# Performance work log

Hardware: AMD Instinct MI355X
Metric: run time of the kernel (lower is better)

## Reference

```python
import jax, jax.numpy as jnp
import numpy as np

N = 200000      # nodes per graph
E = 6400000     # edges per graph
F_IN = 100      # node feature dim (GCNConv(100,16))
HID = 16
NC = 2
STRIDE = 20     # log_softmax(...)[::20]
M = N // STRIDE # rows fed to the MLP head


def _gcn(x, src, dst, W1, b1, W2, b2):
    """PyG-style GCNConv x2: add self loops, sym-normalize, linear -> aggregate -> bias."""
    n = x.shape[0]
    loops = jnp.arange(n)
    s = jnp.concatenate([src, loops])
    d = jnp.concatenate([dst, loops])
    deg = jax.ops.segment_sum(jnp.ones(s.shape[0], dtype=x.dtype), d, num_segments=n)
    dinv = jnp.where(deg > 0, jax.lax.rsqrt(deg), 0.0)
    norm = (dinv[s] * dinv[d])[:, None]  # [E+n, 1]
    h = x @ W1                                    # [n, 16]
    h = jax.ops.segment_sum(norm * h[s], d, num_segments=n) + b1
    h = jax.nn.relu(h)  # dropout is identity in eval mode
    h = h @ W2                                    # [n, 2]
    h = jax.ops.segment_sum(norm * h[s], d, num_segments=n) + b2
    return jax.nn.log_softmax(h, axis=1)[::STRIDE]  # [n/20, 2]


def setup_inputs() -> dict:
    key = jax.random.key(0)
    ks = jax.random.split(key, 24)
    inp = {
        'batch1_edge_index': jax.random.randint(ks[0], (2, E), 0, N),
        'batch1_x': jax.random.normal(ks[1], (N, F_IN), dtype=jnp.float32),
        'batch2_edge_index': jax.random.randint(ks[2], (2, E), 0, N),
        'batch2_x': jax.random.normal(ks[3], (N, F_IN), dtype=jnp.float32),
        'transE_input': jax.random.uniform(ks[4], (M,), dtype=jnp.float32),
        'ComplEx_input': jax.random.uniform(ks[5], (M,), dtype=jnp.float32),
        'path_input': jax.random.uniform(ks[6], (M,), dtype=jnp.float32),
        'edit_input': jax.random.uniform(ks[7], (M,), dtype=jnp.float32),
    }
    s = 0.1
    inp['gh_W1'] = jax.random.normal(ks[8], (F_IN, HID), dtype=jnp.float32) * s
    inp['gh_b1'] = jnp.zeros((HID,), dtype=jnp.float32)
    inp['gh_W2'] = jax.random.normal(ks[9], (HID, NC), dtype=jnp.float32) * s
    inp['gh_b2'] = jnp.zeros((NC,), dtype=jnp.float32)
    inp['gt_W1'] = jax.random.normal(ks[10], (F_IN, HID), dtype=jnp.float32) * s
    inp['gt_b1'] = jnp.zeros((HID,), dtype=jnp.float32)
    inp['gt_W2'] = jax.random.normal(ks[11], (HID, NC), dtype=jnp.float32) * s
    inp['gt_b2'] = jnp.zeros((NC,), dtype=jnp.float32)
    inp['m_W1'] = jax.random.normal(ks[12], (5, 80), dtype=jnp.float32) * s
    inp['m_b1'] = jnp.zeros((80,), dtype=jnp.float32)
    inp['m_W2'] = jax.random.normal(ks[13], (80, 10), dtype=jnp.float32) * s
    inp['m_b2'] = jnp.zeros((10,), dtype=jnp.float32)
    inp['m_W3'] = jax.random.normal(ks[14], (10, 1), dtype=jnp.float32) * s
    inp['m_b3'] = jnp.zeros((1,), dtype=jnp.float32)
    return inp


def reference(batch1_edge_index, batch1_x, batch2_edge_index, batch2_x,
              transE_input, ComplEx_input, path_input, edit_input,
              gh_W1, gh_b1, gh_W2, gh_b2,
              gt_W1, gt_b1, gt_W2, gt_b2,
              m_W1, m_b1, m_W2, m_b2, m_W3, m_b3):
    gcnh_out = _gcn(batch1_x, batch1_edge_index[0], batch1_edge_index[1],
                    gh_W1, gh_b1, gh_W2, gh_b2)
    # gcnt_out is computed in the original forward but never used in the output
    gcnt_out = _gcn(batch2_x, batch2_edge_index[0], batch2_edge_index[1],
                    gt_W1, gt_b1, gt_W2, gt_b2)
    BP_input = jnp.concatenate(
        [transE_input[:, None], ComplEx_input[:, None], path_input[:, None], gcnh_out], axis=1)  # [M, 5]
    # NOTE: original computes mean/std normalization then OVERWRITES it with
    # min_max_normalize(BP_input); we faithfully apply only global min-max.
    mn, mx = jnp.min(BP_input), jnp.max(BP_input)
    BP_norm = (BP_input - mn) / (mx - mn)
    h = jax.nn.relu(BP_norm @ m_W1 + m_b1)
    h = jax.nn.relu(h @ m_W2 + m_b2)
    out = jax.nn.sigmoid(h @ m_W3 + m_b3)  # [M, 1]
    return out
```

## Files before the change

kernel.cpp:

```cpp
#include <hip/hip_runtime.h>
#include <math.h>

#define NN 200000
#define NE 6400000
#define FIN 100
#define MR 10000
#define BSH 14
#define NBK 13
#define NSB 1563
#define EPB 4096
#define STCAP 6144

static __device__ __forceinline__ unsigned enc_f(float f){
  unsigned u = __float_as_uint(f);
  return (u & 0x80000000u) ? ~u : (u | 0x80000000u);
}
static __device__ __forceinline__ float dec_f(unsigned u){
  return (u & 0x80000000u) ? __uint_as_float(u ^ 0x80000000u) : __uint_as_float(~u);
}
static __device__ __forceinline__ unsigned short f2bf(float f){
  unsigned u = __float_as_uint(f);
  return (unsigned short)((u + 0x7fffu + ((u >> 16) & 1u)) >> 16);
}
static __device__ __forceinline__ float bf2f(unsigned short h){
  return __uint_as_float(((unsigned)h) << 16);
}

__global__ void k_init(int* bcnt2, float* gacc, unsigned* mm){
  int i = blockIdx.x*blockDim.x + threadIdx.x;
  if(i < NSB) bcnt2[i] = 0;
  if(i < 2*MR) gacc[i] = 0.f;
  if(i == 0){ mm[0] = 0xFFFFFFFFu; mm[1] = 0u; }
}

__global__ __launch_bounds__(256) void k_hist(const int4* __restrict__ dst4,
                                              int* __restrict__ bcnt2){
  __shared__ int sh[NSB];
  for(int i=threadIdx.x;i<NSB;i+=256) sh[i]=0;
  __syncthreads();
  const int nq = NE/4;
  for(int q = blockIdx.x*256 + threadIdx.x; q < nq; q += gridDim.x*256){
    int4 d = dst4[q];
    atomicAdd(&sh[d.x>>7],1); atomicAdd(&sh[d.y>>7],1);
    atomicAdd(&sh[d.z>>7],1); atomicAdd(&sh[d.w>>7],1);
  }
  __syncthreads();
  for(int i=threadIdx.x;i<NSB;i+=256){ int v=sh[i]; if(v) atomicAdd(&bcnt2[i],v); }
}

__global__ void k_scan2(const int* __restrict__ bcnt2, int* bbase2, int* bcur2,
                        int* bbase1, int* bcur1){
  __shared__ int part[256];
  int t = threadIdx.x;
  int base = t*7;
  int loc[7]; int s = 0;
  #pragma unroll
  for(int j=0;j<7;j++){ int i = base+j; loc[j] = (i<NSB)? bcnt2[i] : 0; s += loc[j]; }
  part[t] = s; __syncthreads();
  for(int o=1;o<256;o<<=1){
    int x = (t>=o)? part[t-o] : 0;
    __syncthreads();
    part[t] += x;
    __syncthreads();
  }
  int run = part[t] - s;
  #pragma unroll
  for(int j=0;j<7;j++){
    int i = base+j;
    if(i<NSB){ bbase2[i] = run; bcur2[i] = run; }
    run += loc[j];
  }
  if(t==0) bbase2[NSB] = NE;
  __syncthreads();
  if(t < NBK){ int v = bbase2[t*128]; bbase1[t] = v; bcur1[t] = v; }
  if(t == NBK){ bbase1[NBK] = NE; }
}

__global__ __launch_bounds__(256) void k_stageA(const int* __restrict__ src,
                                                const int* __restrict__ dst,
                                                int* __restrict__ bcur1,
                                                unsigned* __restrict__ bucket1){
  __shared__ unsigned stage[EPB];
  __shared__ unsigned char binOf[EPB];
  __shared__ int cnt[NBK], bst[NBK], gbase[NBK];
  int t = threadIdx.x;
  int ebase = blockIdx.x*EPB;
  int nEdge = min(EPB, NE - ebase);
  if(t < NBK) cnt[t] = 0;
  __syncthreads();
  unsigned pk[16]; int bb[16], rr[16];
  const int4* s4 = (const int4*)(src + ebase);
  const int4* d4 = (const int4*)(dst + ebase);
  #pragma unroll
  for(int j=0;j<4;j++){
    int q = t + j*256, eo = q*4;
    if(eo < nEdge){
      int4 s = s4[q]; int4 d = d4[q];
      int ds[4] = {d.x,d.y,d.z,d.w}, ss[4] = {s.x,s.y,s.z,s.w};
      #pragma unroll
      for(int k=0;k<4;k++){
        int b = ds[k]>>BSH;
        pk[j*4+k] = ((unsigned)(ds[k] & 16383) << 18) | (unsigned)ss[k];
        bb[j*4+k] = b;
        rr[j*4+k] = atomicAdd(&cnt[b], 1);
      }
    } else {
      rr[j*4+0]=rr[j*4+1]=rr[j*4+2]=rr[j*4+3] = -1;
    }
  }
  __syncthreads();
  if(t == 0){
    int run = 0;
    #pragma unroll
    for(int b=0;b<NBK;b++){ bst[b] = run; run += cnt[b]; }
  }
  __syncthreads();
  if(t < NBK && cnt[t]) gbase[t] = atomicAdd(&bcur1[t], cnt[t]);
  #pragma unroll
  for(int j=0;j<16;j++){
    if(rr[j] >= 0){
      int p = bst[bb[j]] + rr[j];
      stage[p] = pk[j]; binOf[p] = (unsigned char)bb[j];
    }
  }
  __syncthreads();
  for(int k=t; k<nEdge; k+=256){
    int b = binOf[k];
    bucket1[gbase[b] + (k - bst[b])] = stage[k];
  }
}

__global__ __launch_bounds__(256) void k_stageB(const unsigned* __restrict__ bucket1,
                                                const int* __restrict__ bbase1,
                                                int* __restrict__ bcur2,
                                                unsigned* __restrict__ bucket2){
  __shared__ unsigned stage[EPB];
  __shared__ unsigned char binOf[EPB];
  __shared__ int cnt[256], bst[256], gbase[256];
  __shared__ int bb1[NBK+1];
  int t = threadIdx.x;
  int ebase = blockIdx.x*EPB;
  int nEdge = min(EPB, NE - ebase);
  if(t < NBK) bb1[t] = bbase1[t];
  if(t == NBK) bb1[NBK] = NE;
  cnt[t] = 0;
  __syncthreads();
  int bF = 0;
  while(bF < NBK-1 && bb1[bF+1] <= ebase) bF++;
  int sb0 = bF << 7;
  unsigned pk[16]; int ln[16], rr[16];
  const uint4* e4 = (const uint4*)(bucket1 + ebase);
  int b = bF;
  #pragma unroll
  for(int j=0;j<4;j++){
    int q = t + j*256, eo = q*4;
    if(eo < nEdge){
      uint4 e = e4[q];
      unsigned ev[4] = {e.x, e.y, e.z, e.w};
      #pragma unroll
      for(int k=0;k<4;k++){
        int gidx = ebase + eo + k;
        while(b < NBK-1 && bb1[b+1] <= gidx) b++;
        unsigned p = ev[k];
        unsigned dl14 = p >> 18;
        int sbl = ((b<<7) | (int)(dl14>>7)) - sb0;
        pk[j*4+k] = ((dl14 & 127u) << 18) | (p & 0x3FFFFu);
        ln[j*4+k] = sbl;
        rr[j*4+k] = atomicAdd(&cnt[sbl], 1);
      }
    } else {
      rr[j*4+0]=rr[j*4+1]=rr[j*4+2]=rr[j*4+3] = -1;
    }
  }
  __syncthreads();
  if(t == 0){
    int run = 0;
    for(int i=0;i<256;i++){ bst[i] = run; run += cnt[i]; }
  }
  __syncthreads();
  {
    int sbg = sb0 + t;
    if(cnt[t] && sbg < NSB) gbase[t] = atomicAdd(&bcur2[sbg], cnt[t]);
  }
  #pragma unroll
  for(int j=0;j<16;j++){
    if(rr[j] >= 0){
      int p = bst[ln[j]] + rr[j];
      stage[p] = pk[j]; binOf[p] = (unsigned char)ln[j];
    }
  }
  __syncthreads();
  for(int k=t; k<nEdge; k+=256){
    int bin = binOf[k];
    bucket2[gbase[bin] + (k - bst[bin])] = stage[k];
  }
}

__global__ __launch_bounds__(256) void k_cnt(const unsigned* __restrict__ bucket2,
                                             const int* __restrict__ bbase2,
                                             float* __restrict__ dinv){
  __shared__ int c[128];
  int sb = blockIdx.x, t = threadIdx.x;
  if(t < 128) c[t] = 0;
  __syncthreads();
  int e0 = bbase2[sb], e1 = bbase2[sb+1];
  for(int i=e0+t; i<e1; i+=256){
    unsigned pkv = bucket2[i];
    atomicAdd(&c[pkv>>18], 1);
  }
  __syncthreads();
  if(t < 128){
    int g = sb*128 + t;
    if(g < NN) dinv[g] = rsqrtf((float)(c[t] + 1));
  }
}

__global__ __launch_bounds__(256) void k_xw1(const float* __restrict__ x,
                                             const float* __restrict__ W1,
                                             const float* __restrict__ dinv,
                                             unsigned short* __restrict__ h1b){
  int row = blockIdx.x*256 + threadIdx.x;
  if(row >= NN) return;
  const float4* xr = (const float4*)(x + (size_t)row*FIN);
  float acc[16];
  #pragma unroll
  for(int c=0;c<16;c++) acc[c] = 0.f;
  #pragma unroll 5
  for(int kk=0;kk<25;kk++){
    float4 xv = xr[kk];
    const float* w = W1 + kk*4*16;
    #pragma unroll
    for(int c=0;c<16;c++){
      acc[c] += xv.x*w[c] + xv.y*w[16+c] + xv.z*w[32+c] + xv.w*w[48+c];
    }
  }
  float dv = dinv[row];
  unsigned p[8];
  #pragma unroll
  for(int c=0;c<8;c++){
    p[c] = (unsigned)f2bf(acc[2*c]*dv) | ((unsigned)f2bf(acc[2*c+1]*dv) << 16);
  }
  uint4* o = (uint4*)(h1b + (size_t)row*16);
  o[0] = make_uint4(p[0],p[1],p[2],p[3]);
  o[1] = make_uint4(p[4],p[5],p[6],p[7]);
}

__global__ __launch_bounds__(512) void k_aggfused(const unsigned* __restrict__ bucket2,
                                                  const int* __restrict__ bbase2,
                                                  const float* __restrict__ dinv,
                                                  const unsigned short* __restrict__ h1b,
                                                  const float* __restrict__ b1,
                                                  const float* __restrict__ W2,
                                                  float* __restrict__ h2s){
  __shared__ unsigned srt[STCAP];
  __shared__ int cnt[128], coff[129], cur[128];
  __shared__ int wsum0;
  int t = threadIdx.x, sb = blockIdx.x;
  int e0 = bbase2[sb], e1 = bbase2[sb+1];
  int n  = e1 - e0;
  bool ok = (n <= STCAP);
  int grp = t>>4, f = t&15;
  if(t < 128) cnt[t] = 0;
  __syncthreads();

  if(ok){
    for(int i=e0+t; i<e1; i+=512) atomicAdd(&cnt[bucket2[i]>>18], 1);
    __syncthreads();
    int v = (t<128) ? cnt[t] : 0;
    int s = v;
    #pragma unroll
    for(int o=1;o<64;o<<=1){
      int u = __shfl_up(s, o, 64);
      if((t&63) >= o) s += u;
    }
    if(t == 63) wsum0 = s;
    __syncthreads();
    if(t < 128){
      int ex = s - v + ((t>=64) ? wsum0 : 0);
      coff[t] = ex; cur[t] = ex;
    }
    if(t == 0) coff[128] = n;
    __syncthreads();
    for(int i=e0+t; i<e1; i+=512){
      unsigned pkv = bucket2[i];
      int p = atomicAdd(&cur[pkv>>18], 1);
      srt[p] = pkv & 0x3FFFFu;
    }
    __syncthreads();
    for(int nd=grp; nd<128; nd+=32){
      int g = sb*128 + nd;
      if(g >= NN) continue;
      int s0 = coff[nd], s1 = coff[nd+1];
      float acc = bf2f(h1b[(size_t)g*16 + f]);
      int j = s0;
      for(; j+4 <= s1; j+=4){
        unsigned a0=srt[j], a1=srt[j+1], a2=srt[j+2], a3=srt[j+3];
        float x0 = bf2f(h1b[a0*16 + f]);
        float x1 = bf2f(h1b[a1*16 + f]);
        float x2 = bf2f(h1b[a2*16 + f]);
        float x3 = bf2f(h1b[a3*16 + f]);
        acc += (x0+x1) + (x2+x3);
      }
      for(; j<s1; j++) acc += bf2f(h1b[srt[j]*16 + f]);
      float dvd = dinv[g];
      float r = fmaxf(dvd*acc + b1[f], 0.f);
      float p0 = r * W2[f*2+0];
      float p1 = r * W2[f*2+1];
      #pragma unroll
      for(int o=8;o>0;o>>=1){
        p0 += __shfl_xor(p0, o, 16);
        p1 += __shfl_xor(p1, o, 16);
      }
      if(f == 0){
        h2s[g*2+0] = dvd * p0;
        h2s[g*2+1] = dvd * p1;
      }
    }
  } else {
    float* accf = (float*)srt;
    for(int i=t; i<2048; i+=512) accf[i] = 0.f;
    __syncthreads();
    for(int i=e0+grp; i<e1; i+=32){
      unsigned pkv = bucket2[i];
      atomicAdd(&accf[(pkv>>18)*16 + f], bf2f(h1b[(pkv & 0x3FFFFu)*16 + f]));
    }
    __syncthreads();
    for(int nd=grp; nd<128; nd+=32){
      int g = sb*128 + nd;
      if(g >= NN) continue;
      float dvd = dinv[g];
      float acc = accf[nd*16 + f] + bf2f(h1b[(size_t)g*16 + f]);
      float r = fmaxf(dvd*acc + b1[f], 0.f);
      float p0 = r * W2[f*2+0];
      float p1 = r * W2[f*2+1];
      #pragma unroll
      for(int o=8;o>0;o>>=1){
        p0 += __shfl_xor(p0, o, 16);
        p1 += __shfl_xor(p1, o, 16);
      }
      if(f == 0){
        h2s[g*2+0] = dvd * p0;
        h2s[g*2+1] = dvd * p1;
      }
    }
  }
}

__global__ __launch_bounds__(256) void k_agg2e(const unsigned* __restrict__ bucket2,
                                               const int* __restrict__ bbase2,
                                               const float* __restrict__ h2s,
                                               float* __restrict__ gacc){
  int sb = blockIdx.x, t = threadIdx.x;
  int e0 = bbase2[sb], e1 = bbase2[sb+1];
  int base = sb*128;
  for(int i=e0+t; i<e1; i+=256){
    unsigned pkv = bucket2[i];
    int g = base + (int)(pkv >> 18);
    if(g % 20 == 0){
      int srcn = (int)(pkv & 0x3FFFFu);
      int idx = g / 20;
      atomicAdd(&gacc[idx*2+0], h2s[srcn*2+0]);
      atomicAdd(&gacc[idx*2+1], h2s[srcn*2+1]);
    }
  }
}

__global__ __launch_bounds__(256) void k_post(const float* __restrict__ gacc,
                                              const float* __restrict__ h2s,
                                              const float* __restrict__ dinv,
                                              const float* __restrict__ b2,
                                              const float* __restrict__ t1,
                                              const float* __restrict__ t2,
                                              const float* __restrict__ t3,
                                              float* __restrict__ gout,
                                              unsigned* __restrict__ mm){
  int i = blockIdx.x*256 + threadIdx.x;
  float lo = 3.4e38f, hi = -3.4e38f;
  if(i < MR){
    int g = i*20;
    float dvd = dinv[g];
    float o0 = dvd*(gacc[i*2+0] + h2s[g*2+0]) + b2[0];
    float o1 = dvd*(gacc[i*2+1] + h2s[g*2+1]) + b2[1];
    float m = fmaxf(o0, o1);
    float lse = m + logf(expf(o0-m) + expf(o1-m));
    float g0 = o0 - lse, g1 = o1 - lse;
    gout[i*2+0] = g0; gout[i*2+1] = g1;
    float a = t1[i], bb = t2[i], c = t3[i];
    lo = fminf(fminf(a,bb), fminf(c, fminf(g0,g1)));
    hi = fmaxf(fmaxf(a,bb), fmaxf(c, fmaxf(g0,g1)));
  }
  #pragma unroll
  for(int o=32;o>0;o>>=1){
    lo = fminf(lo, __shfl_xor(lo, o, 64));
    hi = fmaxf(hi, __shfl_xor(hi, o, 64));
  }
  __shared__ float slo[4], shi[4];
  int w = threadIdx.x >> 6, l = threadIdx.x & 63;
  if(l == 0){ slo[w] = lo; shi[w] = hi; }
  __syncthreads();
  if(threadIdx.x == 0){
    for(int j=1;j<4;j++){ lo = fminf(lo, slo[j]); hi = fmaxf(hi, shi[j]); }
    atomicMin(&mm[0], enc_f(lo));
    atomicMax(&mm[1], enc_f(hi));
  }
}

__global__ __launch_bounds__(256) void k_mlp(const float* __restrict__ t1, const float* __restrict__ t2,
                                             const float* __restrict__ t3, const float* __restrict__ g,
                                             const unsigned* __restrict__ mm,
                                             const float* __restrict__ W1, const float* __restrict__ b1,
                                             const float* __restrict__ W2, const float* __restrict__ b2,
                                             const float* __restrict__ W3, const float* __restrict__ b3,
                                             float* __restrict__ out){
  int i = blockIdx.x*256 + threadIdx.x;
  if(i >= MR) return;
  float mn = dec_f(mm[0]), mx = dec_f(mm[1]);
  float sc = 1.f/(mx - mn);
  float in[5];
  in[0] = (t1[i]   - mn)*sc;
  in[1] = (t2[i]   - mn)*sc;
  in[2] = (t3[i]   - mn)*sc;
  in[3] = (g[2*i]  - mn)*sc;
  in[4] = (g[2*i+1]- mn)*sc;
  float a[80];
  #pragma unroll
  for(int j=0;j<80;j++){
    float s = b1[j];
    #pragma unroll
    for(int k=0;k<5;k++) s += in[k]*W1[k*80+j];
    a[j] = fmaxf(s, 0.f);
  }
  float h[10];
  #pragma unroll
  for(int j=0;j<10;j++){
    float s = b2[j];
    #pragma unroll
    for(int k=0;k<80;k++) s += a[k]*W2[k*10+j];
    h[j] = fmaxf(s, 0.f);
  }
  float o = b3[0];
  #pragma unroll
  for(int k=0;k<10;k++) o += h[k]*W3[k];
  out[i] = 1.f/(1.f + expf(-o));
}

extern "C" void kernel_launch(void* const* d_in, const int* in_sizes, int n_in,
                              void* d_out, int out_size, void* d_ws, size_t ws_size,
                              hipStream_t stream) {
  (void)in_sizes; (void)n_in; (void)out_size; (void)ws_size;
  const int*   eidx    = (const int*)  d_in[0];
  const int*   src     = eidx;
  const int*   dst     = eidx + NE;
  const int4*  dst4    = (const int4*) dst;
  const float* x       = (const float*)d_in[1];
  const float* transE  = (const float*)d_in[4];
  const float* ComplEx = (const float*)d_in[5];
  const float* path    = (const float*)d_in[6];
  const float* ghW1    = (const float*)d_in[8];
  const float* ghb1    = (const float*)d_in[9];
  const float* ghW2    = (const float*)d_in[10];
  const float* ghb2    = (const float*)d_in[11];
  const float* mW1     = (const float*)d_in[16];
  const float* mb1     = (const float*)d_in[17];
  const float* mW2     = (const float*)d_in[18];
  const float* mb2     = (const float*)d_in[19];
  const float* mW3     = (const float*)d_in[20];
  const float* mb3     = (const float*)d_in[21];
  float* out = (float*)d_out;

  char* w = (char*)d_ws;
  size_t off = 0;
  auto alloc = [&](size_t bytes)->void*{
    void* p = w + off;
    off += (bytes + 255) & ~(size_t)255;
    return p;
  };
  unsigned* bucket1 = (unsigned*)alloc((size_t)NE*4);
  unsigned* bucket2 = (unsigned*)alloc((size_t)NE*4);
  float*    dinv    = (float*)   alloc((size_t)NN*4);
  unsigned short* h1b = (unsigned short*)alloc((size_t)NN*16*2);
  float*    h2s     = (float*)   alloc((size_t)NN*2*4);
  float*    gacc    = (float*)   alloc((size_t)MR*2*4);
  float*    gout    = (float*)   alloc((size_t)MR*2*4);
  int*      bcnt2   = (int*)     alloc((size_t)(NSB+1)*4);
  int*      bbase2  = (int*)     alloc((size_t)(NSB+1)*4);
  int*      bcur2   = (int*)     alloc((size_t)(NSB+1)*4);
  int*      bbase1  = (int*)     alloc(64*4);
  int*      bcur1   = (int*)     alloc(64*4);
  unsigned* mm      = (unsigned*)alloc(256);

  const int SB_BLOCKS = (NE + EPB - 1)/EPB;

  k_init    <<<(2*MR+255)/256, 256, 0, stream>>>(bcnt2, gacc, mm);
  k_hist    <<<1024, 256, 0, stream>>>(dst4, bcnt2);
  k_scan2   <<<1, 256, 0, stream>>>(bcnt2, bbase2, bcur2, bbase1, bcur1);
  k_stageA  <<<SB_BLOCKS, 256, 0, stream>>>(src, dst, bcur1, bucket1);
  k_stageB  <<<SB_BLOCKS, 256, 0, stream>>>(bucket1, bbase1, bcur2, bucket2);
  k_cnt     <<<NSB, 256, 0, stream>>>(bucket2, bbase2, dinv);
  k_xw1     <<<(NN+255)/256, 256, 0, stream>>>(x, ghW1, dinv, h1b);
  k_aggfused<<<NSB, 512, 0, stream>>>(bucket2, bbase2, dinv, h1b, ghb1, ghW2, h2s);
  k_agg2e   <<<NSB, 256, 0, stream>>>(bucket2, bbase2, h2s, gacc);
  k_post    <<<(MR+255)/256, 256, 0, stream>>>(gacc, h2s, dinv, ghb2,
                                               transE, ComplEx, path, gout, mm);
  k_mlp     <<<(MR+255)/256, 256, 0, stream>>>(transE, ComplEx, path, gout, mm,
                                               mW1, mb1, mW2, mb2, mW3, mb3, out);
}
```

Before: 458.5 us.

## Fuse degree count with X·W1, extract sampled edges during partition, replace LDS atomics

In stage A, per-bucket shared-memory atomics are replaced with wave ballot/popcount ranking. The same pass extracts the edges whose destination is a sampled (every-20th) node into a compact global list, so the final second-layer aggregation reads about 320K edges instead of rescanning all 6.4M bucketed edges. The degree count and the X·W1 projection are fused into one kernel that tiles 128 rows of x and all of W1 through shared memory, with two threads per row. The trade-offs are a fixed sample buffer capacity, a 13-bin ballot loop per edge, and heavy LDS use (~58KB) in the fused kernel, which limits occupancy.

```diff
diff --git a/kernel.cpp b/kernel.cpp
--- a/kernel.cpp
+++ b/kernel.cpp
@@ -10,6 +10,8 @@
 #define NSB 1563
 #define EPB 4096
 #define STCAP 6144
+#define SAMPCAP 1024
+#define SAMPG_CAP (1<<20)
 
 static __device__ __forceinline__ unsigned enc_f(float f){
   unsigned u = __float_as_uint(f);
@@ -26,11 +28,11 @@
   return __uint_as_float(((unsigned)h) << 16);
 }
 
-__global__ void k_init(int* bcnt2, float* gacc, unsigned* mm){
+__global__ void k_init(int* bcnt2, float* gacc, unsigned* mm, int* sampCnt){
   int i = blockIdx.x*blockDim.x + threadIdx.x;
   if(i < NSB) bcnt2[i] = 0;
   if(i < 2*MR) gacc[i] = 0.f;
-  if(i == 0){ mm[0] = 0xFFFFFFFFu; mm[1] = 0u; }
+  if(i == 0){ mm[0] = 0xFFFFFFFFu; mm[1] = 0u; sampCnt[0] = 0; }
 }
 
 __global__ __launch_bounds__(256) void k_hist(const int4* __restrict__ dst4,
@@ -79,51 +81,105 @@
 __global__ __launch_bounds__(256) void k_stageA(const int* __restrict__ src,
                                                 const int* __restrict__ dst,
                                                 int* __restrict__ bcur1,
-                                                unsigned* __restrict__ bucket1){
+                                                unsigned* __restrict__ bucket1,
+                                                int* __restrict__ sampCnt,
+                                                unsigned* __restrict__ sampG){
   __shared__ unsigned stage[EPB];
   __shared__ unsigned char binOf[EPB];
-  __shared__ int cnt[NBK], bst[NBK], gbase[NBK];
-  int t = threadIdx.x;
+  __shared__ unsigned samp[SAMPCAP];
+  __shared__ int wtot[4][16], woff[4][16], bst[16], cnt16[16], gbase[16];
+  __shared__ int scnt, sbase;
+  int t = threadIdx.x, lane = t & 63, wv = t >> 6;
   int ebase = blockIdx.x*EPB;
   int nEdge = min(EPB, NE - ebase);
-  if(t < NBK) cnt[t] = 0;
-  __syncthreads();
-  unsigned pk[16]; int bb[16], rr[16];
+  if(t == 0) scnt = 0;
+  __syncthreads();
+
   const int4* s4 = (const int4*)(src + ebase);
   const int4* d4 = (const int4*)(dst + ebase);
+  unsigned pk[16]; int bb[16]; int posw[16];
+  int wcnt[13];
+  #pragma unroll
+  for(int b=0;b<13;b++) wcnt[b]=0;
+  unsigned long long lt = (1ull<<lane)-1ull;
+
   #pragma unroll
   for(int j=0;j<4;j++){
     int q = t + j*256, eo = q*4;
     if(eo < nEdge){
       int4 s = s4[q]; int4 d = d4[q];
-      int ds[4] = {d.x,d.y,d.z,d.w}, ss[4] = {s.x,s.y,s.z,s.w};
+      int ds[4]={d.x,d.y,d.z,d.w}, ss[4]={s.x,s.y,s.z,s.w};
       #pragma unroll
       for(int k=0;k<4;k++){
-        int b = ds[k]>>BSH;
-        pk[j*4+k] = ((unsigned)(ds[k] & 16383) << 18) | (unsigned)ss[k];
-        bb[j*4+k] = b;
-        rr[j*4+k] = atomicAdd(&cnt[b], 1);
+        int r = j*4+k;
+        bb[r] = ds[k]>>BSH;
+        pk[r] = ((unsigned)(ds[k] & 16383) << 18) | (unsigned)ss[k];
       }
     } else {
-      rr[j*4+0]=rr[j*4+1]=rr[j*4+2]=rr[j*4+3] = -1;
-    }
-  }
+      bb[j*4+0]=bb[j*4+1]=bb[j*4+2]=bb[j*4+3] = 15;
+    }
+  }
+  #pragma unroll
+  for(int r=0;r<16;r++){
+    int br = bb[r];
+    #pragma unroll
+    for(int b=0;b<13;b++){
+      unsigned long long m = __ballot(br==b);
+      if(br==b) posw[r] = wcnt[b] + (int)__popcll(m & lt);
+      wcnt[b] += (int)__popcll(m);
+    }
+  }
+  #pragma unroll
+  for(int b=0;b<13;b++) if(lane==b) wtot[wv][b] = wcnt[b];
   __syncthreads();
   if(t == 0){
     int run = 0;
     #pragma unroll
-    for(int b=0;b<NBK;b++){ bst[b] = run; run += cnt[b]; }
-  }
-  __syncthreads();
-  if(t < NBK && cnt[t]) gbase[t] = atomicAdd(&bcur1[t], cnt[t]);
-  #pragma unroll
-  for(int j=0;j<16;j++){
-    if(rr[j] >= 0){
-      int p = bst[bb[j]] + rr[j];
-      stage[p] = pk[j]; binOf[p] = (unsigned char)bb[j];
-    }
-  }
-  __syncthreads();
+    for(int b=0;b<13;b++){
+      int c0=wtot[0][b], c1=wtot[1][b], c2=wtot[2][b], c3=wtot[3][b];
+      int tot = c0+c1+c2+c3;
+      cnt16[b]=tot; bst[b]=run;
+      woff[0][b]=run; woff[1][b]=run+c0; woff[2][b]=run+c0+c1; woff[3][b]=run+c0+c1+c2;
+      run += tot;
+    }
+  }
+  __syncthreads();
+  if(t < NBK && cnt16[t]) gbase[t] = atomicAdd(&bcur1[t], cnt16[t]);
+  #pragma unroll
+  for(int r=0;r<16;r++){
+    if(bb[r] < 13){
+      int p = woff[wv][bb[r]] + posw[r];
+      stage[p] = pk[r]; binOf[p] = (unsigned char)bb[r];
+    }
+  }
+  #pragma unroll
+  for(int r=0;r<16;r++){
+    int dg = (bb[r]<<BSH) | (int)(pk[r]>>18);
+    bool sp = (bb[r] < 13) && (dg % 20 == 0);
+    unsigned long long m = __ballot(sp);
+    if(m){
+      int ldr = __ffsll((unsigned long long)m) - 1;
+      int wb = 0;
+      if(lane == ldr) wb = atomicAdd(&scnt, (int)__popcll(m));
+      wb = __shfl(wb, ldr);
+      if(sp){
+        int p = wb + (int)__popcll(m & lt);
+        unsigned enc2 = ((unsigned)(dg/20) << 18) | (pk[r] & 0x3FFFFu);
+        if(p < SAMPCAP) samp[p] = enc2;
+        else { int gp = atomicAdd(sampCnt, 1); if(gp < SAMPG_CAP) sampG[gp] = enc2; }
+      }
+    }
+  }
+  __syncthreads();
+  if(t == 0) sbase = atomicAdd(sampCnt, min(scnt, SAMPCAP));
+  __syncthreads();
+  {
+    int nS = min(scnt, SAMPCAP);
+    for(int k=t; k<nS; k+=256){
+      int gp = sbase + k;
+      if(gp < SAMPG_CAP) sampG[gp] = samp[k];
+    }
+  }
   for(int k=t; k<nEdge; k+=256){
     int b = binOf[k];
     bucket1[gbase[b] + (k - bst[b])] = stage[k];
@@ -196,53 +252,56 @@
   }
 }
 
-__global__ __launch_bounds__(256) void k_cnt(const unsigned* __restrict__ bucket2,
-                                             const int* __restrict__ bbase2,
-                                             float* __restrict__ dinv){
+__global__ __launch_bounds__(256) void k_cntxw1(const unsigned* __restrict__ bucket2,
+                                                const int* __restrict__ bbase2,
+                                                const float* __restrict__ x,
+                                                const float* __restrict__ W1,
+                                                float* __restrict__ dinv,
+                                                unsigned short* __restrict__ h1b){
+  __shared__ float xs[128*101];
+  __shared__ float w1s[FIN*16];
   __shared__ int c[128];
-  int sb = blockIdx.x, t = threadIdx.x;
+  int t = threadIdx.x, sb = blockIdx.x;
+  int row0 = sb*128;
+  int nrow = min(128, NN - row0);
+  for(int i=t; i<FIN*16; i+=256) w1s[i] = W1[i];
   if(t < 128) c[t] = 0;
   __syncthreads();
   int e0 = bbase2[sb], e1 = bbase2[sb+1];
-  for(int i=e0+t; i<e1; i+=256){
-    unsigned pkv = bucket2[i];
-    atomicAdd(&c[pkv>>18], 1);
-  }
-  __syncthreads();
-  if(t < 128){
-    int g = sb*128 + t;
-    if(g < NN) dinv[g] = rsqrtf((float)(c[t] + 1));
-  }
-}
-
-__global__ __launch_bounds__(256) void k_xw1(const float* __restrict__ x,
-                                             const float* __restrict__ W1,
-                                             const float* __restrict__ dinv,
-                                             unsigned short* __restrict__ h1b){
-  int row = blockIdx.x*256 + threadIdx.x;
-  if(row >= NN) return;
-  const float4* xr = (const float4*)(x + (size_t)row*FIN);
-  float acc[16];
-  #pragma unroll
-  for(int c=0;c<16;c++) acc[c] = 0.f;
-  #pragma unroll 5
-  for(int kk=0;kk<25;kk++){
-    float4 xv = xr[kk];
-    const float* w = W1 + kk*4*16;
-    #pragma unroll
-    for(int c=0;c<16;c++){
-      acc[c] += xv.x*w[c] + xv.y*w[16+c] + xv.z*w[32+c] + xv.w*w[48+c];
-    }
-  }
-  float dv = dinv[row];
-  unsigned p[8];
-  #pragma unroll
-  for(int c=0;c<8;c++){
-    p[c] = (unsigned)f2bf(acc[2*c]*dv) | ((unsigned)f2bf(acc[2*c+1]*dv) << 16);
-  }
-  uint4* o = (uint4*)(h1b + (size_t)row*16);
-  o[0] = make_uint4(p[0],p[1],p[2],p[3]);
-  o[1] = make_uint4(p[4],p[5],p[6],p[7]);
+  for(int i=e0+t; i<e1; i+=256) atomicAdd(&c[bucket2[i]>>18], 1);
+  {
+    const float4* xg = (const float4*)x;
+    int n4 = nrow*25;
+    for(int i=t; i<n4; i+=256){
+      float4 v = xg[row0*25 + i];
+      int r = i/25, c4 = i - r*25;
+      float* p = &xs[r*101 + c4*4];
+      p[0]=v.x; p[1]=v.y; p[2]=v.z; p[3]=v.w;
+    }
+  }
+  __syncthreads();
+  int r = t >> 1, half = t & 1;
+  if(r < nrow){
+    float dv = rsqrtf((float)(c[r] + 1));
+    if(half == 0) dinv[row0 + r] = dv;
+    float acc[8];
+    #pragma unroll
+    for(int j=0;j<8;j++) acc[j] = 0.f;
+    const float* xr = &xs[r*101];
+    #pragma unroll 4
+    for(int k=0;k<FIN;k++){
+      float xv = xr[k];
+      const float* w = &w1s[k*16 + half*8];
+      #pragma unroll
+      for(int j=0;j<8;j++) acc[j] += xv * w[j];
+    }
+    unsigned p[4];
+    #pragma unroll
+    for(int j=0;j<4;j++){
+      p[j] = (unsigned)f2bf(acc[2*j]*dv) | ((unsigned)f2bf(acc[2*j+1]*dv) << 16);
+    }
+    ((uint4*)(h1b + (size_t)(row0+r)*16))[half] = make_uint4(p[0],p[1],p[2],p[3]);
+  }
 }
 
 __global__ __launch_bounds__(512) void k_aggfused(const unsigned* __restrict__ bucket2,
@@ -346,22 +405,17 @@
   }
 }
 
-__global__ __launch_bounds__(256) void k_agg2e(const unsigned* __restrict__ bucket2,
-                                               const int* __restrict__ bbase2,
-                                               const float* __restrict__ h2s,
-                                               float* __restrict__ gacc){
-  int sb = blockIdx.x, t = threadIdx.x;
-  int e0 = bbase2[sb], e1 = bbase2[sb+1];
-  int base = sb*128;
-  for(int i=e0+t; i<e1; i+=256){
-    unsigned pkv = bucket2[i];
-    int g = base + (int)(pkv >> 18);
-    if(g % 20 == 0){
-      int srcn = (int)(pkv & 0x3FFFFu);
-      int idx = g / 20;
-      atomicAdd(&gacc[idx*2+0], h2s[srcn*2+0]);
-      atomicAdd(&gacc[idx*2+1], h2s[srcn*2+1]);
-    }
+__global__ __launch_bounds__(256) void k_gacc(const unsigned* __restrict__ sampG,
+                                              const int* __restrict__ sampCnt,
+                                              const float* __restrict__ h2s,
+                                              float* __restrict__ gacc){
+  int n = min(sampCnt[0], SAMPG_CAP);
+  for(int i = blockIdx.x*256 + threadIdx.x; i < n; i += gridDim.x*256){
+    unsigned e = sampG[i];
+    int s   = (int)(e & 0x3FFFFu);
+    int idx = (int)(e >> 18);
+    atomicAdd(&gacc[idx*2+0], h2s[s*2+0]);
+    atomicAdd(&gacc[idx*2+1], h2s[s*2+1]);
   }
 }
 
@@ -488,20 +542,21 @@
   int*      bbase1  = (int*)     alloc(64*4);
   int*      bcur1   = (int*)     alloc(64*4);
   unsigned* mm      = (unsigned*)alloc(256);
+  int*      sampCnt = (int*)     alloc(256);
+  unsigned* sampG   = (unsigned*)alloc((size_t)SAMPG_CAP*4);
 
   const int SB_BLOCKS = (NE + EPB - 1)/EPB;
 
-  k_init    <<<(2*MR+255)/256, 256, 0, stream>>>(bcnt2, gacc, mm);
-  k_hist    <<<1024, 256, 0, stream>>>(dst4, bcnt2);
-  k_scan2   <<<1, 256, 0, stream>>>(bcnt2, bbase2, bcur2, bbase1, bcur1);
-  k_stageA  <<<SB_BLOCKS, 256, 0, stream>>>(src, dst, bcur1, bucket1);
-  k_stageB  <<<SB_BLOCKS, 256, 0, stream>>>(bucket1, bbase1, bcur2, bucket2);
-  k_cnt     <<<NSB, 256, 0, stream>>>(bucket2, bbase2, dinv);
-  k_xw1     <<<(NN+255)/256, 256, 0, stream>>>(x, ghW1, dinv, h1b);
+  k_init   <<<(2*MR+255)/256, 256, 0, stream>>>(bcnt2, gacc, mm, sampCnt);
+  k_hist   <<<1024, 256, 0, stream>>>(dst4, bcnt2);
+  k_scan2  <<<1, 256, 0, stream>>>(bcnt2, bbase2, bcur2, bbase1, bcur1);
+  k_stageA <<<SB_BLOCKS, 256, 0, stream>>>(src, dst, bcur1, bucket1, sampCnt, sampG);
+  k_stageB <<<SB_BLOCKS, 256, 0, stream>>>(bucket1, bbase1, bcur2, bucket2);
+  k_cntxw1 <<<NSB, 256, 0, stream>>>(bucket2, bbase2, x, ghW1, dinv, h1b);
   k_aggfused<<<NSB, 512, 0, stream>>>(bucket2, bbase2, dinv, h1b, ghb1, ghW2, h2s);
-  k_agg2e   <<<NSB, 256, 0, stream>>>(bucket2, bbase2, h2s, gacc);
-  k_post    <<<(MR+255)/256, 256, 0, stream>>>(gacc, h2s, dinv, ghb2,
-                                               transE, ComplEx, path, gout, mm);
-  k_mlp     <<<(MR+255)/256, 256, 0, stream>>>(transE, ComplEx, path, gout, mm,
-                                               mW1, mb1, mW2, mb2, mW3, mb3, out);
-}
+  k_gacc   <<<512, 256, 0, stream>>>(sampG, sampCnt, h2s, gacc);
+  k_post   <<<(MR+255)/256, 256, 0, stream>>>(gacc, h2s, dinv, ghb2,
+                                              transE, ComplEx, path, gout, mm);
+  k_mlp    <<<(MR+255)/256, 256, 0, stream>>>(transE, ComplEx, path, gout, mm,
+                                              mW1, mb1, mW2, mb2, mW3, mb3, out);
+}
```

Measured after the change: 523.5 us. +14.2%, slower.
